# Optimization experiments

Hardware: AMD Instinct MI355X
Metric: run time of the kernel (lower is better)

Reference implementation:

```python
import jax, jax.numpy as jnp
import numpy as np
from jax import lax

EPS = 1e-5


def binarize(x):
    return jnp.sign(x)


def conv3x3(x, w):
    # x: NCHW, w: OIHW, stride 1, padding 1 (SAME for k=3)
    return lax.conv_general_dilated(
        x, w, window_strides=(1, 1), padding=((1, 1), (1, 1)),
        dimension_numbers=("NCHW", "OIHW", "NCHW"))


def prelu(x, a):
    # a broadcastable per-channel slope
    return jnp.where(x >= 0, x, a * x)


def bn(x, gamma, beta, axes):
    mean = jnp.mean(x, axis=axes, keepdims=True)
    var = jnp.var(x, axis=axes, keepdims=True)
    shp = [1] * x.ndim
    shp[1] = x.shape[1]
    g = gamma.reshape(shp)
    b = beta.reshape(shp)
    return (x - mean) * lax.rsqrt(var + EPS) * g + b


def setup_inputs() -> dict:
    key = jax.random.key(0)
    ks = jax.random.split(key, 8)
    B = 256
    C = [1, 64, 128]
    FC_IN = 28 * 28 * C[-1]  # 100352
    F1, F2 = 1024, 10
    inp = {
        "x": jax.random.normal(ks[0], (B, C[0], 28, 28), jnp.float32),
        "cw0": jax.random.normal(ks[1], (C[1], C[0], 3, 3), jnp.float32) * 0.1,
        "cp0": jnp.full((C[1],), 0.25, jnp.float32),
        "cg0": jnp.ones((C[1],), jnp.float32),
        "cb0": jnp.zeros((C[1],), jnp.float32),
        "cw1": jax.random.normal(ks[2], (C[2], C[1], 3, 3), jnp.float32) * 0.1,
        "cp1": jnp.full((C[2],), 0.25, jnp.float32),
        "cg1": jnp.ones((C[2],), jnp.float32),
        "cb1": jnp.zeros((C[2],), jnp.float32),
        "fw0": jax.random.normal(ks[3], (F1, FC_IN), jnp.float32) * 0.02,
        "fp0": jnp.full((F1,), 0.25, jnp.float32),
        "fg0": jnp.ones((F1,), jnp.float32),
        "fb0": jnp.zeros((F1,), jnp.float32),
        "fw1": jax.random.normal(ks[4], (F2, F1), jnp.float32) * 0.05,
        "fp1": jnp.full((F2,), 0.25, jnp.float32),
        "fg1": jnp.ones((F2,), jnp.float32),
        "fb1": jnp.zeros((F2,), jnp.float32),
        "scale": jnp.ones((1,), jnp.float32),
    }
    return inp


def reference(x, cw0, cp0, cg0, cb0, cw1, cp1, cg1, cb1,
              fw0, fp0, fg0, fb0, fw1, fp1, fg1, fb1, scale):
    # conv block 0
    h = binarize(x)
    h = conv3x3(h, jnp.sign(cw0))
    h = prelu(h, cp0[None, :, None, None])
    h = bn(h, cg0, cb0, axes=(0, 2, 3))
    # conv block 1
    h = binarize(h)
    h = conv3x3(h, jnp.sign(cw1))
    h = prelu(h, cp1[None, :, None, None])
    h = bn(h, cg1, cb1, axes=(0, 2, 3))
    # flatten
    h = h.reshape(-1, 28 * 28 * cw1.shape[0])
    # fc block 0
    h = binarize(h)
    h = h @ jnp.sign(fw0).T
    h = prelu(h, fp0[None, :])
    h = bn(h, fg0, fb0, axes=(0,))
    # fc block 1
    h = binarize(h)
    h = h @ jnp.sign(fw1).T
    h = prelu(h, fp1[None, :])
    h = bn(h, fg1, fb1, axes=(0,))
    # scale layer
    return h * scale
```

## Files before the change

kernel.cpp:

```cpp
#include <hip/hip_runtime.h>
#include <stdint.h>


static constexpr int BATCH = 256;
static constexpr int K0    = 100352;
static constexpr int KW    = 1568;
static constexpr int N1    = 1024;
static constexpr int KS2   = 49;
static constexpr int JW2   = 32;
static constexpr int SUB2  = 8;
static constexpr int NS2   = 4;
static constexpr unsigned ZCAP = 65536;

__device__ __forceinline__ float fsign(float v){
    return (v > 0.f) ? 1.f : ((v < 0.f) ? -1.f : 0.f);
}

__global__ __launch_bounds__(256) void k_pack_w1(const float* __restrict__ cw1,
        uint64_t* __restrict__ wn1, uint64_t* __restrict__ wnz1,
        int* __restrict__ zero_region)
{
    if (blockIdx.x == 0) {
        for (int i = threadIdx.x; i < 832; i += 256) zero_region[i] = 0;
    }
    int idx = blockIdx.x*4 + (threadIdx.x >> 6);
    int lane = threadIdx.x & 63;
    int oc = idx / 9, t = idx % 9;
    float w = cw1[oc*576 + lane*9 + t];
    uint64_t n = __ballot(w < 0.f);
    uint64_t z = __ballot(w != 0.f);
    if (lane == 0) { wn1[idx] = n; wnz1[idx] = z; }
}

__global__ __launch_bounds__(256) void k_conv0(const float* __restrict__ x,
        const float* __restrict__ cw0, const float* __restrict__ cp0,
        int8_t* __restrict__ h0s, double* __restrict__ S0, double* __restrict__ Q0)
{
    __shared__ float img[30][30];
    __shared__ float redS[4][64];
    __shared__ float redQ[4][64];
    int b = blockIdx.x;
    int tid = threadIdx.x;
    for (int i = tid; i < 900; i += 256) ((float*)img)[i] = 0.f;
    __syncthreads();
    for (int i = tid; i < 784; i += 256) {
        float v = x[b*784 + i];
        img[1 + i/28][1 + i%28] = fsign(v);
    }
    __syncthreads();
    int lane = tid & 63, wv = tid >> 6;
    float wsg[9];
    #pragma unroll
    for (int t = 0; t < 9; t++) wsg[t] = fsign(cw0[lane*9 + t]);
    float a = cp0[lane];
    float accS = 0.f, accQ = 0.f;
    for (int i = 0; i < 196; i++) {
        int p = wv*196 + i;
        int y = p / 28, xx = p % 28;
        float s = 0.f;
        #pragma unroll
        for (int dy = 0; dy < 3; dy++)
            #pragma unroll
            for (int dx = 0; dx < 3; dx++)
                s += img[y+dy][xx+dx] * wsg[dy*3+dx];
        h0s[(size_t)(b*784 + p)*64 + lane] = (int8_t)(int)s;
        float v = (s >= 0.f) ? s : a*s;
        accS += v; accQ += v*v;
    }
    redS[wv][lane] = accS; redQ[wv][lane] = accQ;
    __syncthreads();
    if (tid < 64) {
        double s = (double)redS[0][tid] + redS[1][tid] + redS[2][tid] + redS[3][tid];
        double q = (double)redQ[0][tid] + redQ[1][tid] + redQ[2][tid] + redQ[3][tid];
        atomicAdd(&S0[tid], s);
        atomicAdd(&Q0[tid], q);
    }
}

__global__ void k_bnfin0(const double* __restrict__ S, const double* __restrict__ Q,
        const float* __restrict__ g, const float* __restrict__ bb,
        const float* __restrict__ cp0, unsigned* __restrict__ lut)
{
    int c = threadIdx.x;
    double mean = S[c] * (1.0/200704.0);
    double var  = Q[c] * (1.0/200704.0) - mean*mean;
    if (var < 0.0) var = 0.0;
    double A = (double)g[c] / sqrt(var + 1e-5);
    double B = (double)bb[c] - mean*A;
    float a = cp0[c];
    unsigned m = 0;
    for (int s = -9; s <= 9; ++s) {
        float v = (s >= 0) ? (float)s : a*(float)s;
        double t = fma((double)v, A, B);
        if (t < 0.0) m |= 1u << (s + 9);
    }
    lut[c] = m;
}

__global__ void k_bnfin(const double* __restrict__ S, const double* __restrict__ Q,
        const float* __restrict__ g, const float* __restrict__ bb,
        double* __restrict__ AB, int C, double invN)
{
    int c = threadIdx.x;
    if (c >= C) return;
    double mean = S[c] * invN;
    double var  = Q[c] * invN - mean*mean;
    if (var < 0.0) var = 0.0;
    double A = (double)g[c] / sqrt(var + 1e-5);
    AB[c]     = A;
    AB[C + c] = (double)bb[c] - mean*A;
}

__global__ __launch_bounds__(256) void k_pack_h0(const int8_t* __restrict__ h0s,
        const unsigned* __restrict__ lut, uint64_t* __restrict__ hp)
{
    __shared__ unsigned l[64];
    int tid = threadIdx.x;
    if (tid < 64) l[tid] = lut[tid];
    __syncthreads();
    int pixel = blockIdx.x*256 + tid;
    const int4* p4 = (const int4*)(h0s + (size_t)pixel*64);
    int4 va = p4[0], vb = p4[1], vc = p4[2], vd = p4[3];
    int wa[16] = {va.x,va.y,va.z,va.w, vb.x,vb.y,vb.z,vb.w,
                  vc.x,vc.y,vc.z,vc.w, vd.x,vd.y,vd.z,vd.w};
    unsigned lo = 0, hi = 0;
    #pragma unroll
    for (int wi = 0; wi < 16; ++wi) {
        unsigned w = (unsigned)wa[wi];
        #pragma unroll
        for (int c2 = 0; c2 < 4; ++c2) {
            int ch = wi*4 + c2;
            int s = (int)(signed char)(w >> (8*c2));
            unsigned bit = (l[ch] >> (s + 9)) & 1u;
            if (ch < 32) lo |= bit << ch; else hi |= bit << (ch - 32);
        }
    }
    hp[pixel] = ((uint64_t)hi << 32) | lo;
}

__global__ __launch_bounds__(256) void k_conv1(const uint64_t* __restrict__ hp,
        const uint64_t* __restrict__ wn1, const uint64_t* __restrict__ wnz1,
        const float* __restrict__ cp1, int16_t* __restrict__ h1s,
        double* __restrict__ S1, double* __restrict__ Q1)
{
    __shared__ float lS[4][8];
    __shared__ float lQ[4][8];
    int bid = blockIdx.x;
    int ocg = bid & 15;
    int ptg = (bid >> 4) & 3;
    int b   = bid >> 6;
    int wv = threadIdx.x >> 6, lane = threadIdx.x & 63;
    int pt = ptg*4 + wv;
    bool active = (pt < 13);
    int p = active ? (pt*64 + lane) : 0;
    bool pvalid = active && (p < 784);
    int y = p / 28, xx = p % 28;
    uint64_t nb[9]; unsigned vmask = 0;
    #pragma unroll
    for (int dy = 0; dy < 3; dy++)
        #pragma unroll
        for (int dx = 0; dx < 3; dx++) {
            int t = dy*3+dx;
            int yy = y + dy - 1, xv = xx + dx - 1;
            bool ok = (yy >= 0 && yy < 28 && xv >= 0 && xv < 28);
            nb[t] = hp[b*784 + (ok ? (yy*28+xv) : 0)];
            if (ok) vmask |= 1u << t;
        }
    #pragma unroll
    for (int o = 0; o < 8; o++) {
        int oc = ocg*8 + o;
        int base = oc*9;
        int acc = 0;
        #pragma unroll
        for (int t = 0; t < 9; t++) {
            uint64_t wn = wn1[base+t], wz = wnz1[base+t];
            if (vmask & (1u<<t))
                acc += (int)__popcll(wz) - 2*(int)__popcll((nb[t] ^ wn) & wz);
        }
        if (pvalid) h1s[((size_t)b*128 + oc)*784 + p] = (int16_t)acc;
        float pr = cp1[oc];
        float v = pvalid ? ((acc >= 0) ? (float)acc : pr*(float)acc) : 0.f;
        float s = v, q = v*v;
        #pragma unroll
        for (int off = 32; off; off >>= 1) {
            s += __shfl_xor(s, off);
            q += __shfl_xor(q, off);
        }
        if (lane == 0) { lS[wv][o] = s; lQ[wv][o] = q; }
    }
    __syncthreads();
    if (threadIdx.x < 8) {
        int o = threadIdx.x;
        double s = (double)lS[0][o] + lS[1][o] + lS[2][o] + lS[3][o];
        double q = (double)lQ[0][o] + lQ[1][o] + lQ[2][o] + lQ[3][o];
        atomicAdd(&S1[ocg*8 + o], s);
        atomicAdd(&Q1[ocg*8 + o], q);
    }
}

__global__ __launch_bounds__(256) void k_pack_a0(const int16_t* __restrict__ h1s,
        const float* __restrict__ cp1, const double* __restrict__ AB,
        uint64_t* __restrict__ ap_t)
{
    int blk = blockIdx.x;
    int b  = blk / 98;
    int qg = blk % 98;
    int wv = threadIdx.x >> 6, lane = threadIdx.x & 63;
    int q  = qg*4 + wv;
    int k0 = q*256 + lane*4;
    short4 sv = *(const short4*)(h1s + (size_t)b*K0 + k0);
    int oc = k0 / 784;
    double A = AB[oc], B = AB[128 + oc];
    float a = cp1[oc];
    int ss[4] = {sv.x, sv.y, sv.z, sv.w};
    uint64_t words[4];
    #pragma unroll
    for (int c = 0; c < 4; ++c) {
        float s = (float)ss[c];
        float v = (s >= 0.f) ? s : a*s;
        double t = fma((double)v, A, B);
        words[c] = __ballot(t < 0.0);
    }
    if (lane == 0) {
        #pragma unroll
        for (int c = 0; c < 4; ++c)
            ap_t[(size_t)(4*q + c)*256 + b] = words[c];
    }
}

__global__ __launch_bounds__(256) void k_pack_w0(const float* __restrict__ fw0,
        uint64_t* __restrict__ wp, unsigned* __restrict__ zcnt,
        uint64_t* __restrict__ zlist)
{
    int n   = blockIdx.x >> 1;
    int oct = (blockIdx.x & 1)*4 + (threadIdx.x >> 6);
    int lane = threadIdx.x & 63;
    const float* src = fw0 + (size_t)n*K0 + (size_t)oct*49*256 + lane*4;
    uint64_t* dst = wp + (size_t)n*KW + (size_t)oct*49*4;
    for (int t = 0; t < 49; ++t) {
        float4 w = *(const float4*)(src + t*256);
        uint64_t g0 = __ballot(w.x < 0.f);
        uint64_t g1 = __ballot(w.y < 0.f);
        uint64_t g2 = __ballot(w.z < 0.f);
        uint64_t g3 = __ballot(w.w < 0.f);
        uint64_t z0 = __ballot(w.x == 0.f);
        uint64_t z1 = __ballot(w.y == 0.f);
        uint64_t z2 = __ballot(w.z == 0.f);
        uint64_t z3 = __ballot(w.w == 0.f);
        if (lane == 0) {
            ulonglong2 lo{g0, g1}, hi{g2, g3};
            *(ulonglong2*)(dst + t*4)     = lo;
            *(ulonglong2*)(dst + t*4 + 2) = hi;
            uint64_t zz[4] = {z0, z1, z2, z3};
            #pragma unroll
            for (int c = 0; c < 4; ++c) if (zz[c]) {
                unsigned id = atomicAdd(zcnt, 1u);
                if (id < ZCAP) {
                    unsigned j = (unsigned)((oct*49 + t)*4 + c);
                    zlist[2*id]   = ((uint64_t)(unsigned)n << 32) | j;
                    zlist[2*id+1] = zz[c];
                }
            }
        }
    }
}

__global__ __launch_bounds__(256) void k_fc0g(const uint64_t* __restrict__ wp,
        const uint64_t* __restrict__ ap_t, int16_t* __restrict__ pcpart)
{
    __shared__ uint64_t wT[32][33];
    __shared__ uint64_t apL[SUB2][256];
    int nt = blockIdx.x & 31;
    int ks = blockIdx.x >> 5;
    int tid = threadIdx.x;
    int bq = tid & 31;
    int nq = tid >> 5;
    int n0 = nt*32, j0 = ks*JW2;
    {
        int row = tid >> 3;
        int wo  = (tid & 7) * 4;
        const uint64_t* src = wp + (size_t)(n0 + row)*KW + j0 + wo;
        ulonglong2 v0 = *(const ulonglong2*)(src);
        ulonglong2 v1 = *(const ulonglong2*)(src + 2);
        wT[row][wo+0] = v0.x; wT[row][wo+1] = v0.y;
        wT[row][wo+2] = v1.x; wT[row][wo+3] = v1.y;
    }
    int pc[8][4];
    #pragma unroll
    for (int i = 0; i < 8; i++)
        #pragma unroll
        for (int k = 0; k < 4; k++) pc[i][k] = 0;
    for (int c = 0; c < NS2; c++) {
        #pragma unroll
        for (int r = 0; r < SUB2; r++)
            apL[r][tid] = ap_t[(size_t)(j0 + c*SUB2 + r)*256 + tid];
        __syncthreads();
        #pragma unroll
        for (int jj = 0; jj < SUB2; jj++) {
            uint64_t aw[8], ww[4];
            #pragma unroll
            for (int i = 0; i < 8; i++) aw[i] = apL[jj][bq + 32*i];
            #pragma unroll
            for (int k = 0; k < 4; k++) ww[k] = wT[nq + 8*k][c*8 + jj];
            #pragma unroll
            for (int i = 0; i < 8; i++)
                #pragma unroll
                for (int k = 0; k < 4; k++)
                    pc[i][k] += (int)__popcll(aw[i] ^ ww[k]);
        }
        __syncthreads();
    }
    #pragma unroll
    for (int k = 0; k < 4; k++) {
        int n = n0 + nq + 8*k;
        #pragma unroll
        for (int i = 0; i < 8; i++)
            pcpart[((size_t)ks*N1 + n)*BATCH + (bq + 32*i)] = (int16_t)pc[i][k];
    }
}

__global__ __launch_bounds__(256) void k_fc0ep(const int16_t* __restrict__ pcpart,
        const unsigned* __restrict__ zcnt, const uint64_t* __restrict__ zlist,
        const uint64_t* __restrict__ ap_t, const float* __restrict__ fp0,
        const float* __restrict__ fg0, const float* __restrict__ fb0,
        float* __restrict__ af)
{
    int n = blockIdx.x, b = threadIdx.x;
    int pc = 0;
    #pragma unroll
    for (int ks = 0; ks < KS2; ks++) pc += (int)pcpart[((size_t)ks*N1 + n)*BATCH + b];
    int s = K0 - 2*pc;
    unsigned cnt = *zcnt; if (cnt > ZCAP) cnt = ZCAP;
    for (unsigned e = 0; e < cnt; ++e) {
        uint64_t key = zlist[2*e];
        if ((int)(key >> 32) == n) {
            uint64_t zm = zlist[2*e+1];
            uint64_t a = ap_t[(size_t)(key & 0xffffffffu)*256 + b];
            s += 2*(int)__popcll(a & zm) - (int)__popcll(zm);
        }
    }
    float a = fp0[n];
    float v = (s >= 0) ? (float)s : a*(float)s;
    __shared__ double rs[256], rq[256];
    rs[b] = v; rq[b] = (double)v*(double)v;
    __syncthreads();
    for (int off=128; off>0; off>>=1){
        if (b<off){ rs[b]+=rs[b+off]; rq[b]+=rq[b+off]; }
        __syncthreads();
    }
    __shared__ double AB[2];
    if (b == 0) {
        double mean = rs[0] / 256.0;
        double var = rq[0] / 256.0 - mean*mean;
        if (var < 0.0) var = 0.0;
        double A = (double)fg0[n] / sqrt(var + 1e-5);
        AB[0] = A; AB[1] = (double)fb0[n] - mean*A;
    }
    __syncthreads();
    double t = fma((double)v, AB[0], AB[1]);
    af[(size_t)n*256 + b] = (t > 0.0) ? 1.f : ((t < 0.0) ? -1.f : 0.f);
}

__global__ __launch_bounds__(256) void k_fc1a(const float* __restrict__ af,
        const float* __restrict__ fw1, float* __restrict__ part9)
{
    __shared__ float swL[10][32];
    int ks = blockIdx.x, b = threadIdx.x;
    for (int i = b; i < 320; i += 256) {
        int j = i / 32, kk = i % 32;
        swL[j][kk] = fsign(fw1[j*1024 + ks*32 + kk]);
    }
    __syncthreads();
    float acc[10];
    #pragma unroll
    for (int j=0;j<10;j++) acc[j]=0.f;
    for (int kk = 0; kk < 32; kk++) {
        float a = af[(size_t)(ks*32+kk)*256 + b];
        #pragma unroll
        for (int j=0;j<10;j++) acc[j] += a * swL[j][kk];
    }
    #pragma unroll
    for (int j=0;j<10;j++) part9[((size_t)ks*256 + b)*10 + j] = acc[j];
}

__global__ __launch_bounds__(256) void k_fc1b(const float* __restrict__ part9,
        const float* __restrict__ fp1, const float* __restrict__ fg1,
        const float* __restrict__ fb1, const float* __restrict__ scale,
        float* __restrict__ out)
{
    int b = threadIdx.x;
    float v[10];
    #pragma unroll
    for (int j=0;j<10;j++) v[j]=0.f;
    for (int ks=0; ks<32; ks++)
        #pragma unroll
        for (int j=0;j<10;j++) v[j] += part9[((size_t)ks*256+b)*10 + j];
    #pragma unroll
    for (int j=0;j<10;j++){
        float a = fp1[j];
        v[j] = (v[j] >= 0.f) ? v[j] : a*v[j];
    }
    __shared__ double sv[256];
    __shared__ double AB[2][10];
    for (int j=0;j<10;j++){
        sv[b] = (double)v[j];
        __syncthreads();
        for (int off=128;off>0;off>>=1){ if(b<off) sv[b]+=sv[b+off]; __syncthreads(); }
        double mean = sv[0]/256.0;
        __syncthreads();
        double d = (double)v[j]-mean;
        sv[b] = d*d;
        __syncthreads();
        for (int off=128;off>0;off>>=1){ if(b<off) sv[b]+=sv[b+off]; __syncthreads(); }
        if (b==0){
            double var = sv[0]/256.0;
            double A = (double)fg1[j]/sqrt(var+1e-5);
            AB[0][j]=A; AB[1][j]=(double)fb1[j] - mean*A;
        }
        __syncthreads();
    }
    float sc = scale[0];
    #pragma unroll
    for (int j=0;j<10;j++)
        out[b*10+j] = (float)fma((double)v[j], AB[0][j], AB[1][j]) * sc;
}

extern "C" void kernel_launch(void* const* d_in, const int* in_sizes, int n_in,
                              void* d_out, int out_size, void* d_ws, size_t ws_size,
                              hipStream_t stream)
{
    const float* x    = (const float*)d_in[0];
    const float* cw0  = (const float*)d_in[1];
    const float* cp0  = (const float*)d_in[2];
    const float* cg0  = (const float*)d_in[3];
    const float* cb0  = (const float*)d_in[4];
    const float* cw1  = (const float*)d_in[5];
    const float* cp1  = (const float*)d_in[6];
    const float* cg1  = (const float*)d_in[7];
    const float* cb1  = (const float*)d_in[8];
    const float* fw0  = (const float*)d_in[9];
    const float* fp0  = (const float*)d_in[10];
    const float* fg0  = (const float*)d_in[11];
    const float* fb0  = (const float*)d_in[12];
    const float* fw1  = (const float*)d_in[13];
    const float* fp1  = (const float*)d_in[14];
    const float* fg1  = (const float*)d_in[15];
    const float* fb1  = (const float*)d_in[16];
    const float* scale= (const float*)d_in[17];

    char* ws = (char*)d_ws;
    size_t off = 0;
    auto alloc = [&](size_t bytes)->char* {
        char* r = ws + off; off = (off + bytes + 255) & ~(size_t)255; return r; };

    double*   S0    = (double*)alloc(64*8);
    double*   Q0    = (double*)alloc(64*8);
    double*   S1    = (double*)alloc(128*8);
    double*   Q1    = (double*)alloc(128*8);
    unsigned* zcnt  = (unsigned*)alloc(256);
    unsigned* lut0  = (unsigned*)alloc(64*4);
    double*   A1B1  = (double*)alloc(256*8);
    int8_t*   h0s   = (int8_t*)alloc((size_t)256*784*64);
    uint64_t* hp    = (uint64_t*)alloc((size_t)256*784*8);
    int16_t*  h1s   = (int16_t*)alloc((size_t)256*128*784*2);
    uint64_t* ap_t  = (uint64_t*)alloc((size_t)KW*256*8);
    uint64_t* wn1   = (uint64_t*)alloc(1152*8);
    uint64_t* wnz1  = (uint64_t*)alloc(1152*8);
    uint64_t* wp    = (uint64_t*)alloc((size_t)N1*KW*8);
    int16_t*  pcpart= (int16_t*)alloc((size_t)KS2*N1*BATCH*2);
    float*    af    = (float*)alloc((size_t)1024*256*4);
    float*    part9 = (float*)alloc((size_t)32*256*10*4);
    uint64_t* zlist = (uint64_t*)alloc((size_t)ZCAP*16);
    (void)ws_size; (void)in_sizes; (void)n_in; (void)out_size;

    k_pack_w1<<<288,   256, 0, stream>>>(cw1, wn1, wnz1, (int*)d_ws);
    k_conv0  <<<256,   256, 0, stream>>>(x, cw0, cp0, h0s, S0, Q0);
    k_bnfin0 <<<1,      64, 0, stream>>>(S0, Q0, cg0, cb0, cp0, lut0);
    k_pack_h0<<<784,   256, 0, stream>>>(h0s, lut0, hp);
    k_conv1  <<<16384, 256, 0, stream>>>(hp, wn1, wnz1, cp1, h1s, S1, Q1);
    k_bnfin  <<<1,     128, 0, stream>>>(S1, Q1, cg1, cb1, A1B1, 128, 1.0/200704.0);
    k_pack_a0<<<256*98,256, 0, stream>>>(h1s, cp1, A1B1, ap_t);
    k_pack_w0<<<2048,  256, 0, stream>>>(fw0, wp, zcnt, zlist);
    k_fc0g   <<<KS2*32,256, 0, stream>>>(wp, ap_t, pcpart);
    k_fc0ep  <<<1024,  256, 0, stream>>>(pcpart, zcnt, zlist, ap_t, fp0, fg0, fb0, af);
    k_fc1a   <<<32,    256, 0, stream>>>(af, fw1, part9);
    k_fc1b   <<<1,     256, 0, stream>>>(part9, fp1, fg1, fb1, scale, (float*)d_out);
}
```

Before: 355.1 us.

## Fuse weight packing into FC GEMM, inline BN finalize, replace conv1 atomics

```diff
diff --git a/kernel.cpp b/kernel.cpp
--- a/kernel.cpp
+++ b/kernel.cpp
@@ -21,7 +21,7 @@
         int* __restrict__ zero_region)
 {
     if (blockIdx.x == 0) {
-        for (int i = threadIdx.x; i < 832; i += 256) zero_region[i] = 0;
+        for (int i = threadIdx.x; i < 512; i += 256) zero_region[i] = 0;
     }
     int idx = blockIdx.x*4 + (threadIdx.x >> 6);
     int lane = threadIdx.x & 63;
@@ -77,46 +77,27 @@
     }
 }
 
-__global__ void k_bnfin0(const double* __restrict__ S, const double* __restrict__ Q,
-        const float* __restrict__ g, const float* __restrict__ bb,
-        const float* __restrict__ cp0, unsigned* __restrict__ lut)
-{
-    int c = threadIdx.x;
-    double mean = S[c] * (1.0/200704.0);
-    double var  = Q[c] * (1.0/200704.0) - mean*mean;
-    if (var < 0.0) var = 0.0;
-    double A = (double)g[c] / sqrt(var + 1e-5);
-    double B = (double)bb[c] - mean*A;
-    float a = cp0[c];
-    unsigned m = 0;
-    for (int s = -9; s <= 9; ++s) {
-        float v = (s >= 0) ? (float)s : a*(float)s;
-        double t = fma((double)v, A, B);
-        if (t < 0.0) m |= 1u << (s + 9);
-    }
-    lut[c] = m;
-}
-
-__global__ void k_bnfin(const double* __restrict__ S, const double* __restrict__ Q,
-        const float* __restrict__ g, const float* __restrict__ bb,
-        double* __restrict__ AB, int C, double invN)
-{
-    int c = threadIdx.x;
-    if (c >= C) return;
-    double mean = S[c] * invN;
-    double var  = Q[c] * invN - mean*mean;
-    if (var < 0.0) var = 0.0;
-    double A = (double)g[c] / sqrt(var + 1e-5);
-    AB[c]     = A;
-    AB[C + c] = (double)bb[c] - mean*A;
-}
-
 __global__ __launch_bounds__(256) void k_pack_h0(const int8_t* __restrict__ h0s,
-        const unsigned* __restrict__ lut, uint64_t* __restrict__ hp)
+        const double* __restrict__ S0, const double* __restrict__ Q0,
+        const float* __restrict__ cg0, const float* __restrict__ cb0,
+        const float* __restrict__ cp0, uint64_t* __restrict__ hp)
 {
     __shared__ unsigned l[64];
     int tid = threadIdx.x;
-    if (tid < 64) l[tid] = lut[tid];
+    if (tid < 64) {
+        double mean = S0[tid] * (1.0/200704.0);
+        double var  = Q0[tid] * (1.0/200704.0) - mean*mean;
+        if (var < 0.0) var = 0.0;
+        double A = (double)cg0[tid] / sqrt(var + 1e-5);
+        double B = (double)cb0[tid] - mean*A;
+        float a = cp0[tid];
+        unsigned m = 0;
+        for (int s = -9; s <= 9; ++s) {
+            float v = (s >= 0) ? (float)s : a*(float)s;
+            if (fma((double)v, A, B) < 0.0) m |= 1u << (s + 9);
+        }
+        l[tid] = m;
+    }
     __syncthreads();
     int pixel = blockIdx.x*256 + tid;
     const int4* p4 = (const int4*)(h0s + (size_t)pixel*64);
@@ -141,7 +122,7 @@
 __global__ __launch_bounds__(256) void k_conv1(const uint64_t* __restrict__ hp,
         const uint64_t* __restrict__ wn1, const uint64_t* __restrict__ wnz1,
         const float* __restrict__ cp1, int16_t* __restrict__ h1s,
-        double* __restrict__ S1, double* __restrict__ Q1)
+        double* __restrict__ pS1, double* __restrict__ pQ1)
 {
     __shared__ float lS[4][8];
     __shared__ float lQ[4][8];
@@ -189,12 +170,41 @@
         if (lane == 0) { lS[wv][o] = s; lQ[wv][o] = q; }
     }
     __syncthreads();
-    if (threadIdx.x < 8) {
-        int o = threadIdx.x;
-        double s = (double)lS[0][o] + lS[1][o] + lS[2][o] + lS[3][o];
-        double q = (double)lQ[0][o] + lQ[1][o] + lQ[2][o] + lQ[3][o];
-        atomicAdd(&S1[ocg*8 + o], s);
-        atomicAdd(&Q1[ocg*8 + o], q);
+    if (threadIdx.x < 16) {
+        int o = threadIdx.x & 7;
+        bool isQ = threadIdx.x >= 8;
+        double v4 = isQ ? ((double)lQ[0][o] + lQ[1][o] + lQ[2][o] + lQ[3][o])
+                        : ((double)lS[0][o] + lS[1][o] + lS[2][o] + lS[3][o]);
+        double* dst = isQ ? pQ1 : pS1;
+        dst[(size_t)(ocg*8 + o)*1024 + (b*4 + ptg)] = v4;
+    }
+}
+
+__global__ __launch_bounds__(256) void k_bnfin1(const double* __restrict__ pS,
+        const double* __restrict__ pQ, const float* __restrict__ g,
+        const float* __restrict__ bb, double* __restrict__ AB)
+{
+    int oc = blockIdx.x;
+    int tid = threadIdx.x;
+    double s = 0.0, q = 0.0;
+    #pragma unroll
+    for (int i = 0; i < 4; ++i) {
+        s += pS[(size_t)oc*1024 + tid + 256*i];
+        q += pQ[(size_t)oc*1024 + tid + 256*i];
+    }
+    __shared__ double rs[256], rq[256];
+    rs[tid] = s; rq[tid] = q;
+    __syncthreads();
+    for (int off = 128; off; off >>= 1) {
+        if (tid < off) { rs[tid] += rs[tid+off]; rq[tid] += rq[tid+off]; }
+        __syncthreads();
+    }
+    if (tid == 0) {
+        double mean = rs[0] * (1.0/200704.0);
+        double var  = rq[0] * (1.0/200704.0) - mean*mean;
+        if (var < 0.0) var = 0.0;
+        double A = (double)g[oc] / sqrt(var + 1e-5);
+        AB[oc] = A; AB[128 + oc] = (double)bb[oc] - mean*A;
     }
 }
 
@@ -228,63 +238,54 @@
     }
 }
 
-__global__ __launch_bounds__(256) void k_pack_w0(const float* __restrict__ fw0,
-        uint64_t* __restrict__ wp, unsigned* __restrict__ zcnt,
-        uint64_t* __restrict__ zlist)
-{
-    int n   = blockIdx.x >> 1;
-    int oct = (blockIdx.x & 1)*4 + (threadIdx.x >> 6);
-    int lane = threadIdx.x & 63;
-    const float* src = fw0 + (size_t)n*K0 + (size_t)oct*49*256 + lane*4;
-    uint64_t* dst = wp + (size_t)n*KW + (size_t)oct*49*4;
-    for (int t = 0; t < 49; ++t) {
-        float4 w = *(const float4*)(src + t*256);
-        uint64_t g0 = __ballot(w.x < 0.f);
-        uint64_t g1 = __ballot(w.y < 0.f);
-        uint64_t g2 = __ballot(w.z < 0.f);
-        uint64_t g3 = __ballot(w.w < 0.f);
-        uint64_t z0 = __ballot(w.x == 0.f);
-        uint64_t z1 = __ballot(w.y == 0.f);
-        uint64_t z2 = __ballot(w.z == 0.f);
-        uint64_t z3 = __ballot(w.w == 0.f);
-        if (lane == 0) {
-            ulonglong2 lo{g0, g1}, hi{g2, g3};
-            *(ulonglong2*)(dst + t*4)     = lo;
-            *(ulonglong2*)(dst + t*4 + 2) = hi;
-            uint64_t zz[4] = {z0, z1, z2, z3};
+__global__ __launch_bounds__(256) void k_fc0g(const float* __restrict__ fw0,
+        const uint64_t* __restrict__ ap_t, int16_t* __restrict__ pcpart,
+        unsigned* __restrict__ zcnt, uint64_t* __restrict__ zlist)
+{
+    __shared__ uint64_t wT[32][33];
+    __shared__ uint64_t apL[SUB2][256];
+    int ks = blockIdx.x % KS2;
+    int nt = blockIdx.x / KS2;
+    int tid = threadIdx.x;
+    int wv = tid >> 6, lane = tid & 63;
+    int n0 = nt*32, j0 = ks*JW2;
+    {
+        const float* wsrc = fw0 + (size_t)(n0 + wv*8)*K0 + (size_t)(ks*8)*256 + lane*4;
+        for (int r8 = 0; r8 < 8; ++r8) {
+            const float* rowp = wsrc + (size_t)r8*K0;
+            int row = wv*8 + r8;
             #pragma unroll
-            for (int c = 0; c < 4; ++c) if (zz[c]) {
-                unsigned id = atomicAdd(zcnt, 1u);
-                if (id < ZCAP) {
-                    unsigned j = (unsigned)((oct*49 + t)*4 + c);
-                    zlist[2*id]   = ((uint64_t)(unsigned)n << 32) | j;
-                    zlist[2*id+1] = zz[c];
+            for (int qq = 0; qq < 8; ++qq) {
+                float4 w = *(const float4*)(rowp + qq*256);
+                uint64_t g0 = __ballot(w.x < 0.f);
+                uint64_t g1 = __ballot(w.y < 0.f);
+                uint64_t g2 = __ballot(w.z < 0.f);
+                uint64_t g3 = __ballot(w.w < 0.f);
+                uint64_t z0 = __ballot(w.x == 0.f);
+                uint64_t z1 = __ballot(w.y == 0.f);
+                uint64_t z2 = __ballot(w.z == 0.f);
+                uint64_t z3 = __ballot(w.w == 0.f);
+                if (lane == 0) {
+                    wT[row][qq*4+0] = g0;
+                    wT[row][qq*4+1] = g1;
+                    wT[row][qq*4+2] = g2;
+                    wT[row][qq*4+3] = g3;
+                    uint64_t zz[4] = {z0, z1, z2, z3};
+                    #pragma unroll
+                    for (int c = 0; c < 4; ++c) if (zz[c]) {
+                        unsigned id = atomicAdd(zcnt, 1u);
+                        if (id < ZCAP) {
+                            unsigned j = (unsigned)((ks*8 + qq)*4 + c);
+                            zlist[2*id]   = ((uint64_t)(unsigned)(n0+row) << 32) | j;
+                            zlist[2*id+1] = zz[c];
+                        }
+                    }
                 }
             }
         }
     }
-}
-
-__global__ __launch_bounds__(256) void k_fc0g(const uint64_t* __restrict__ wp,
-        const uint64_t* __restrict__ ap_t, int16_t* __restrict__ pcpart)
-{
-    __shared__ uint64_t wT[32][33];
-    __shared__ uint64_t apL[SUB2][256];
-    int nt = blockIdx.x & 31;
-    int ks = blockIdx.x >> 5;
-    int tid = threadIdx.x;
     int bq = tid & 31;
     int nq = tid >> 5;
-    int n0 = nt*32, j0 = ks*JW2;
-    {
-        int row = tid >> 3;
-        int wo  = (tid & 7) * 4;
-        const uint64_t* src = wp + (size_t)(n0 + row)*KW + j0 + wo;
-        ulonglong2 v0 = *(const ulonglong2*)(src);
-        ulonglong2 v1 = *(const ulonglong2*)(src + 2);
-        wT[row][wo+0] = v0.x; wT[row][wo+1] = v0.y;
-        wT[row][wo+2] = v1.x; wT[row][wo+3] = v1.y;
-    }
     int pc[8][4];
     #pragma unroll
     for (int i = 0; i < 8; i++)
@@ -455,34 +456,30 @@
 
     double*   S0    = (double*)alloc(64*8);
     double*   Q0    = (double*)alloc(64*8);
-    double*   S1    = (double*)alloc(128*8);
-    double*   Q1    = (double*)alloc(128*8);
     unsigned* zcnt  = (unsigned*)alloc(256);
-    unsigned* lut0  = (unsigned*)alloc(64*4);
     double*   A1B1  = (double*)alloc(256*8);
+    double*   pS1   = (double*)alloc((size_t)128*1024*8);
+    double*   pQ1   = (double*)alloc((size_t)128*1024*8);
     int8_t*   h0s   = (int8_t*)alloc((size_t)256*784*64);
     uint64_t* hp    = (uint64_t*)alloc((size_t)256*784*8);
     int16_t*  h1s   = (int16_t*)alloc((size_t)256*128*784*2);
     uint64_t* ap_t  = (uint64_t*)alloc((size_t)KW*256*8);
     uint64_t* wn1   = (uint64_t*)alloc(1152*8);
     uint64_t* wnz1  = (uint64_t*)alloc(1152*8);
-    uint64_t* wp    = (uint64_t*)alloc((size_t)N1*KW*8);
     int16_t*  pcpart= (int16_t*)alloc((size_t)KS2*N1*BATCH*2);
     float*    af    = (float*)alloc((size_t)1024*256*4);
     float*    part9 = (float*)alloc((size_t)32*256*10*4);
     uint64_t* zlist = (uint64_t*)alloc((size_t)ZCAP*16);
     (void)ws_size; (void)in_sizes; (void)n_in; (void)out_size;
 
-    k_pack_w1<<<288,   256, 0, stream>>>(cw1, wn1, wnz1, (int*)d_ws);
-    k_conv0  <<<256,   256, 0, stream>>>(x, cw0, cp0, h0s, S0, Q0);
-    k_bnfin0 <<<1,      64, 0, stream>>>(S0, Q0, cg0, cb0, cp0, lut0);
-    k_pack_h0<<<784,   256, 0, stream>>>(h0s, lut0, hp);
-    k_conv1  <<<16384, 256, 0, stream>>>(hp, wn1, wnz1, cp1, h1s, S1, Q1);
-    k_bnfin  <<<1,     128, 0, stream>>>(S1, Q1, cg1, cb1, A1B1, 128, 1.0/200704.0);
-    k_pack_a0<<<256*98,256, 0, stream>>>(h1s, cp1, A1B1, ap_t);
-    k_pack_w0<<<2048,  256, 0, stream>>>(fw0, wp, zcnt, zlist);
-    k_fc0g   <<<KS2*32,256, 0, stream>>>(wp, ap_t, pcpart);
-    k_fc0ep  <<<1024,  256, 0, stream>>>(pcpart, zcnt, zlist, ap_t, fp0, fg0, fb0, af);
-    k_fc1a   <<<32,    256, 0, stream>>>(af, fw1, part9);
-    k_fc1b   <<<1,     256, 0, stream>>>(part9, fp1, fg1, fb1, scale, (float*)d_out);
-}
+    k_pack_w1<<<288,     256, 0, stream>>>(cw1, wn1, wnz1, (int*)d_ws);
+    k_conv0  <<<256,     256, 0, stream>>>(x, cw0, cp0, h0s, S0, Q0);
+    k_pack_h0<<<784,     256, 0, stream>>>(h0s, S0, Q0, cg0, cb0, cp0, hp);
+    k_conv1  <<<16384,   256, 0, stream>>>(hp, wn1, wnz1, cp1, h1s, pS1, pQ1);
+    k_bnfin1 <<<128,     256, 0, stream>>>(pS1, pQ1, cg1, cb1, A1B1);
+    k_pack_a0<<<256*98,  256, 0, stream>>>(h1s, cp1, A1B1, ap_t);
+    k_fc0g   <<<KS2*32,  256, 0, stream>>>(fw0, ap_t, pcpart, zcnt, zlist);
+    k_fc0ep  <<<1024,    256, 0, stream>>>(pcpart, zcnt, zlist, ap_t, fp0, fg0, fb0, af);
+    k_fc1a   <<<32,      256, 0, stream>>>(af, fw1, part9);
+    k_fc1b   <<<1,       256, 0, stream>>>(part9, fp1, fg1, fb1, scale, (float*)d_out);
+}
```

Result: no change. 350.6 us (-1.3%).
